# Kernel tuning notes

Measured on AMD Instinct MI355X. Metric: run time of the kernel, lower is better.

The kernel has to match this reference:

```python
import jax, jax.numpy as jnp
import numpy as np

B, C, T_IN, R, TB = 8192, 3, 2048, 64, 128
ALPHA = 10.0  # steepness of sigmoid surrogate spike
Q_INIT = 6.0


def surrogate_spike(x):
    # Differentiable surrogate for the spiking nonlinearity (sigmoid fast-spike).
    return jax.nn.sigmoid(ALPHA * x)


def setup_inputs() -> dict:
    key = jax.random.key(0)
    k0, k1 = jax.random.split(key)
    traces = jax.random.normal(k0, (B, C, T_IN), jnp.float32)
    drive_w = jax.random.normal(k1, (R, C), jnp.float32) / np.sqrt(C)
    drive_b = jnp.zeros((R,), jnp.float32)
    frequency_raw = jnp.linspace(-1.2, 1.2, R, dtype=jnp.float32)
    q_center = float(np.log(np.exp(max(Q_INIT - 1.5, 1e-3)) - 1.0))  # inverse softplus
    q_raw = jnp.full((R,), q_center, jnp.float32)
    threshold_raw = jnp.zeros((R,), jnp.float32)
    return dict(traces=traces, drive_w=drive_w, drive_b=drive_b,
                frequency_raw=frequency_raw, q_raw=q_raw, threshold_raw=threshold_raw)


def reference(traces, drive_w, drive_b, frequency_raw, q_raw, threshold_raw):
    b, c, t = traces.shape
    win = t // TB  # adaptive_avg_pool1d with evenly-dividing window
    pooled = traces.reshape(b, c, TB, win).mean(axis=-1)  # [B, C, TB]
    # _normalize_traces: divide by per-sample max-abs clamped to >= 1
    scale = jnp.maximum(jnp.max(jnp.abs(pooled), axis=(1, 2), keepdims=True), 1.0)
    pooled = pooled / scale
    # 1x1 Conv1d == per-timestep linear projection C -> R
    drive = jnp.einsum('bct,rc->brt', pooled, drive_w) + drive_b[None, :, None]  # [B, R, TB]

    frequency = 0.03 + 0.17 * jax.nn.sigmoid(frequency_raw)      # [R]
    q_factor = 1.5 + jax.nn.softplus(q_raw)                      # [R]
    decay = jnp.exp(-1.0 / q_factor)                             # [R]
    threshold = 0.35 + 0.75 * jax.nn.sigmoid(threshold_raw)      # [R]

    def step(carry, current):
        state, velocity = carry
        velocity = decay * velocity + current - frequency * state
        state = state + frequency * velocity
        spikes = surrogate_spike(state - threshold)
        state = state - spikes * threshold
        return (state, velocity), spikes

    init = (jnp.zeros((b, R), drive.dtype), jnp.zeros((b, R), drive.dtype))
    drive_t = jnp.moveaxis(drive, -1, 0)  # [TB, B, R]
    _, spike_seq = jax.lax.scan(step, init, drive_t)  # spike_seq: [TB, B, R]
    return spike_seq.mean(axis=0)  # [B, R]
```

## Files before the change

### kernel.cpp

```cpp
#include <hip/hip_runtime.h>
#include <math.h>

constexpr int kC   = 3;
constexpr int kTIn = 2048;
constexpr int kR   = 64;
constexpr int kTB  = 128;
constexpr float kAlpha = 10.0f;
constexpr float kLog2e = 1.44269504088896f;

constexpr int kK   = 4;
constexpr int kF4  = kC * kTIn / 4;

#ifndef __has_builtin
#define __has_builtin(x) 0
#endif

static __device__ __forceinline__ float fast_rcp(float x) {
#if __has_builtin(__builtin_amdgcn_rcpf)
    return __builtin_amdgcn_rcpf(x);
#else
    return 1.0f / x;
#endif
}

static __device__ __forceinline__ float fast_exp2(float x) {
#if __has_builtin(__builtin_amdgcn_exp2f)
    return __builtin_amdgcn_exp2f(x);
#else
    return __builtin_exp2f(x);
#endif
}

__global__ __launch_bounds__(256, 8)
void fused_encoder_kernel(const float* __restrict__ traces,
                          const float* __restrict__ drive_w,
                          const float* __restrict__ drive_b,
                          const float* __restrict__ freq_raw,
                          const float* __restrict__ q_raw,
                          const float* __restrict__ thr_raw,
                          float* __restrict__ out)
{
    __shared__ float sp[2][kTB * 4];
    __shared__ float red[2][3];

    const int tid  = threadIdx.x;
    const int wave = tid >> 6;
    const int lane = tid & 63;
    const int scanWave = blockIdx.x & 3;
    const long long base = (long long)blockIdx.x * kK;
    const float4* tr4 = reinterpret_cast<const float4*>(traces);

    if (wave != scanWave) {
        const int h = wave - (wave > scanWave ? 1 : 0);

        auto pool = [&](long long b, int buf) {
            const float4* src = tr4 + b * kF4 + (h * 8) * 64 + lane;
            float mloc = 0.0f;
            #pragma unroll
            for (int j = 0; j < 8; ++j) {
                float4 v = src[j * 64];
                float s = (v.x + v.y) + (v.z + v.w);
                s += __shfl_xor(s, 1, 64);
                s += __shfl_xor(s, 2, 64);
                mloc = fmaxf(mloc, fabsf(s));
                if ((lane & 3) == 0) {
                    int w = (h * 8 + j) * 16 + (lane >> 2);
                    sp[buf][(w & 127) * 4 + (w >> 7)] = s;
                }
            }
            #pragma unroll
            for (int off = 4; off <= 32; off <<= 1)
                mloc = fmaxf(mloc, __shfl_xor(mloc, off, 64));
            if (lane == 0) red[buf][h] = mloc;
        };

        pool(base, 0);
        __syncthreads();
        for (int k = 0; k < kK; ++k) {
            if (k + 1 < kK) pool(base + k + 1, (k + 1) & 1);
            __syncthreads();
        }
    } else {
        const int r = lane;
        const float w0   = drive_w[r * kC + 0];
        const float w1   = drive_w[r * kC + 1];
        const float w2   = drive_w[r * kC + 2];
        const float bias = drive_b[r];
        const float freq  = 0.03f + 0.17f / (1.0f + expf(-freq_raw[r]));
        const float qf    = 1.5f + log1pf(expf(q_raw[r]));
        const float decay = expf(-1.0f / qf);
        const float thr   = 0.35f + 0.75f / (1.0f + expf(-thr_raw[r]));
        const float expScale = kAlpha * kLog2e;
        const float thrE  = thr * expScale;

        __syncthreads();
        for (int k = 0; k < kK; ++k) {
            const int cur = k & 1;
            const float mm = fmaxf(fmaxf(red[cur][0], red[cur][1]), red[cur][2]);
            const float inv = fast_rcp(fmaxf(mm * (1.0f / 16.0f), 1.0f)) * (1.0f / 16.0f);
            const float v0 = w0 * inv, v1 = w1 * inv, v2 = w2 * inv;
            const float4* pt = reinterpret_cast<const float4*>(sp[cur]);

            __builtin_amdgcn_s_setprio(1);
            float state = 0.0f, vel = 0.0f, acc = 0.0f;
            #pragma unroll 8
            for (int t = 0; t < kTB; ++t) {
                float4 p = pt[t];
                float cur_ = fmaf(p.x, v0, bias);
                cur_ = fmaf(p.y, v1, cur_);
                cur_ = fmaf(p.z, v2, cur_);
                vel = fmaf(decay, vel, cur_);
                vel = fmaf(-freq, state, vel);
                state = fmaf(freq, vel, state);
                float e = fast_exp2(fmaf(-expScale, state, thrE));
                float spike = fast_rcp(1.0f + e);
                state = fmaf(-spike, thr, state);
                acc += spike;
            }
            __builtin_amdgcn_s_setprio(0);

            out[(base + k) * kR + r] = acc * (1.0f / kTB);
            __syncthreads();
        }
    }
}

extern "C" void kernel_launch(void* const* d_in, const int* in_sizes, int n_in,
                              void* d_out, int out_size, void* d_ws, size_t ws_size,
                              hipStream_t stream)
{
    const float* traces   = (const float*)d_in[0];
    const float* drive_w  = (const float*)d_in[1];
    const float* drive_b  = (const float*)d_in[2];
    const float* freq_raw = (const float*)d_in[3];
    const float* q_raw    = (const float*)d_in[4];
    const float* thr_raw  = (const float*)d_in[5];
    float* out = (float*)d_out;

    const int totalB = in_sizes[0] / (kC * kTIn);
    const int grid = totalB / kK;

    fused_encoder_kernel<<<grid, 256, 0, stream>>>(traces, drive_w, drive_b,
                                                   freq_raw, q_raw, thr_raw, out);
}
```

Measured before the change: 40.02 us.

## Split wave roles into two scan waves and two pooling waves per block

Each block now runs two scan waves and two pooling waves instead of one scan wave and three pooling waves. Each pooling wave reduces a whole sample, and the two scan waves handle alternate samples from a per-wave double-buffered shared tile. This halves the serial recurrence chain each block must run, which is the latency-bound critical path. In exchange, each pooling wave issues three times as many loads per sample, and shared memory use doubles.

```diff
diff --git a/kernel.cpp b/kernel.cpp
--- a/kernel.cpp
+++ b/kernel.cpp
@@ -40,32 +40,35 @@
                           const float* __restrict__ thr_raw,
                           float* __restrict__ out)
 {
-    __shared__ float sp[2][kTB * 4];
-    __shared__ float red[2][3];
+    __shared__ float sp[2][2][kTB * 4];
+    __shared__ float red[2][2];
 
     const int tid  = threadIdx.x;
     const int wave = tid >> 6;
     const int lane = tid & 63;
-    const int scanWave = blockIdx.x & 3;
+    const int s0 = blockIdx.x & 3;
+    const int s1 = s0 ^ 1;
     const long long base = (long long)blockIdx.x * kK;
     const float4* tr4 = reinterpret_cast<const float4*>(traces);
 
-    if (wave != scanWave) {
-        const int h = wave - (wave > scanWave ? 1 : 0);
+    const bool isScan = (wave == s0) || (wave == s1);
+
+    if (!isScan) {
+        const int h = wave & 1;
 
         auto pool = [&](long long b, int buf) {
-            const float4* src = tr4 + b * kF4 + (h * 8) * 64 + lane;
+            const float4* src = tr4 + b * kF4 + lane;
             float mloc = 0.0f;
             #pragma unroll
-            for (int j = 0; j < 8; ++j) {
+            for (int j = 0; j < 24; ++j) {
                 float4 v = src[j * 64];
                 float s = (v.x + v.y) + (v.z + v.w);
                 s += __shfl_xor(s, 1, 64);
                 s += __shfl_xor(s, 2, 64);
                 mloc = fmaxf(mloc, fabsf(s));
                 if ((lane & 3) == 0) {
-                    int w = (h * 8 + j) * 16 + (lane >> 2);
-                    sp[buf][(w & 127) * 4 + (w >> 7)] = s;
+                    int w = j * 16 + (lane >> 2);
+                    sp[buf][h][(w & 127) * 4 + (w >> 7)] = s;
                 }
             }
             #pragma unroll
@@ -74,13 +77,14 @@
             if (lane == 0) red[buf][h] = mloc;
         };
 
-        pool(base, 0);
+        pool(base + h, 0);
         __syncthreads();
-        for (int k = 0; k < kK; ++k) {
-            if (k + 1 < kK) pool(base + k + 1, (k + 1) & 1);
+        for (int p = 0; p < 2; ++p) {
+            if (p + 1 < 2) pool(base + 2 * (p + 1) + h, (p + 1) & 1);
             __syncthreads();
         }
     } else {
+        const int si = (wave == s1) ? 1 : 0;
         const int r = lane;
         const float w0   = drive_w[r * kC + 0];
         const float w1   = drive_w[r * kC + 1];
@@ -94,21 +98,21 @@
         const float thrE  = thr * expScale;
 
         __syncthreads();
-        for (int k = 0; k < kK; ++k) {
-            const int cur = k & 1;
-            const float mm = fmaxf(fmaxf(red[cur][0], red[cur][1]), red[cur][2]);
+        for (int p = 0; p < 2; ++p) {
+            const int cur = p & 1;
+            const float mm = red[cur][si];
             const float inv = fast_rcp(fmaxf(mm * (1.0f / 16.0f), 1.0f)) * (1.0f / 16.0f);
             const float v0 = w0 * inv, v1 = w1 * inv, v2 = w2 * inv;
-            const float4* pt = reinterpret_cast<const float4*>(sp[cur]);
+            const float4* pt = reinterpret_cast<const float4*>(sp[cur][si]);
 
             __builtin_amdgcn_s_setprio(1);
             float state = 0.0f, vel = 0.0f, acc = 0.0f;
             #pragma unroll 8
             for (int t = 0; t < kTB; ++t) {
-                float4 p = pt[t];
-                float cur_ = fmaf(p.x, v0, bias);
-                cur_ = fmaf(p.y, v1, cur_);
-                cur_ = fmaf(p.z, v2, cur_);
+                float4 pv = pt[t];
+                float cur_ = fmaf(pv.x, v0, bias);
+                cur_ = fmaf(pv.y, v1, cur_);
+                cur_ = fmaf(pv.z, v2, cur_);
                 vel = fmaf(decay, vel, cur_);
                 vel = fmaf(-freq, state, vel);
                 state = fmaf(freq, vel, state);
@@ -119,7 +123,7 @@
             }
             __builtin_amdgcn_s_setprio(0);
 
-            out[(base + k) * kR + r] = acc * (1.0f / kTB);
+            out[(base + 2 * p + si) * kR + r] = acc * (1.0f / kTB);
             __syncthreads();
         }
     }
```

After: 49.55 us. 23.8% more time.

## Persistent grid with async global-to-LDS double-buffered trace loading

Applied to the files above, without the earlier changes.

Switches to a fixed 768-block persistent grid in which each block handles a contiguous range of samples. Raw traces now go straight into LDS through async global_load_lds, double-buffered two samples ahead, and are pooled from shared memory. Synchronisation uses manual s_waitcnt and s_barrier. The aim is to keep more bytes in flight and overlap the memory-bound load with the sequential scan. The cost is large LDS use (about 48KB per block), lower occupancy, and a longer serial scan chain in each block's scan wave.

```diff
diff --git a/kernel.cpp b/kernel.cpp
--- a/kernel.cpp
+++ b/kernel.cpp
@@ -8,8 +8,8 @@
 constexpr float kAlpha = 10.0f;
 constexpr float kLog2e = 1.44269504088896f;
 
-constexpr int kK   = 4;
-constexpr int kF4  = kC * kTIn / 4;
+constexpr int kSampleF = kC * kTIn;
+constexpr int kGrid    = 768;
 
 #ifndef __has_builtin
 #define __has_builtin(x) 0
@@ -31,54 +31,81 @@
 #endif
 }
 
-__global__ __launch_bounds__(256, 8)
+__global__ __launch_bounds__(256, 3)
 void fused_encoder_kernel(const float* __restrict__ traces,
                           const float* __restrict__ drive_w,
                           const float* __restrict__ drive_b,
                           const float* __restrict__ freq_raw,
                           const float* __restrict__ q_raw,
                           const float* __restrict__ thr_raw,
-                          float* __restrict__ out)
+                          float* __restrict__ out,
+                          int kSmall, int rem)
 {
+    __shared__ float raw[2][kSampleF];
     __shared__ float sp[2][kTB * 4];
     __shared__ float red[2][3];
 
     const int tid  = threadIdx.x;
     const int wave = tid >> 6;
     const int lane = tid & 63;
-    const int scanWave = blockIdx.x & 3;
-    const long long base = (long long)blockIdx.x * kK;
-    const float4* tr4 = reinterpret_cast<const float4*>(traces);
 
-    if (wave != scanWave) {
-        const int h = wave - (wave > scanWave ? 1 : 0);
+    const int bx = blockIdx.x;
+    int K; long long base;
+    if (bx < rem) { K = kSmall + 1; base = (long long)bx * K; }
+    else          { K = kSmall;     base = (long long)rem * (kSmall + 1)
+                                         + (long long)(bx - rem) * kSmall; }
 
-        auto pool = [&](long long b, int buf) {
-            const float4* src = tr4 + b * kF4 + (h * 8) * 64 + lane;
+    if (wave < 3) {
+        const int p = wave;
+
+        auto dma = [&](long long s, int buf) {
+            const float* src = traces + s * kSampleF + p * 2048 + lane * 4;
+            float* dst = &raw[buf][p * 2048];
+            #pragma unroll
+            for (int j = 0; j < 8; ++j) {
+                __builtin_amdgcn_global_load_lds(
+                    (const __attribute__((address_space(1))) void*)(src + j * 256),
+                    (__attribute__((address_space(3))) void*)(dst + j * 256),
+                    16, 0, 0);
+            }
+        };
+        auto pool = [&](int buf) {
+            const float4* r4 = reinterpret_cast<const float4*>(raw[buf]);
             float mloc = 0.0f;
             #pragma unroll
-            for (int j = 0; j < 8; ++j) {
-                float4 v = src[j * 64];
+            for (int j2 = 0; j2 < 8; ++j2) {
+                const int j = p * 8 + j2;
+                float4 v = r4[j * 64 + lane];
                 float s = (v.x + v.y) + (v.z + v.w);
                 s += __shfl_xor(s, 1, 64);
                 s += __shfl_xor(s, 2, 64);
                 mloc = fmaxf(mloc, fabsf(s));
                 if ((lane & 3) == 0) {
-                    int w = (h * 8 + j) * 16 + (lane >> 2);
+                    int w = j * 16 + (lane >> 2);
                     sp[buf][(w & 127) * 4 + (w >> 7)] = s;
                 }
             }
             #pragma unroll
             for (int off = 4; off <= 32; off <<= 1)
                 mloc = fmaxf(mloc, __shfl_xor(mloc, off, 64));
-            if (lane == 0) red[buf][h] = mloc;
+            if (lane == 0) red[buf][p] = mloc;
         };
 
-        pool(base, 0);
-        __syncthreads();
-        for (int k = 0; k < kK; ++k) {
-            if (k + 1 < kK) pool(base + k + 1, (k + 1) & 1);
-            __syncthreads();
+        dma(base + 0, 0);
+        if (K > 1) dma(base + 1, 1);
+        asm volatile("s_waitcnt vmcnt(8)" ::: "memory");
+        pool(0);
+        asm volatile("s_waitcnt lgkmcnt(0)\n\ts_barrier" ::: "memory");
+
+        for (int k = 0; k < K; ++k) {
+            if (k + 2 < K) {
+                dma(base + k + 2, k & 1);
+                asm volatile("s_waitcnt vmcnt(8)" ::: "memory");
+            } else {
+                asm volatile("s_waitcnt vmcnt(0)" ::: "memory");
+            }
+            if (k + 1 < K) pool((k + 1) & 1);
+            asm volatile("s_waitcnt lgkmcnt(0)\n\ts_barrier" ::: "memory");
         }
     } else {
         const int r = lane;
@@ -93,8 +120,8 @@
         const float expScale = kAlpha * kLog2e;
         const float thrE  = thr * expScale;
 
-        __syncthreads();
-        for (int k = 0; k < kK; ++k) {
+        asm volatile("s_barrier" ::: "memory");
+        for (int k = 0; k < K; ++k) {
             const int cur = k & 1;
             const float mm = fmaxf(fmaxf(red[cur][0], red[cur][1]), red[cur][2]);
             const float inv = fast_rcp(fmaxf(mm * (1.0f / 16.0f), 1.0f)) * (1.0f / 16.0f);
@@ -105,10 +132,10 @@
             float state = 0.0f, vel = 0.0f, acc = 0.0f;
             #pragma unroll 8
             for (int t = 0; t < kTB; ++t) {
-                float4 p = pt[t];
-                float cur_ = fmaf(p.x, v0, bias);
-                cur_ = fmaf(p.y, v1, cur_);
-                cur_ = fmaf(p.z, v2, cur_);
+                float4 pv = pt[t];
+                float cur_ = fmaf(pv.x, v0, bias);
+                cur_ = fmaf(pv.y, v1, cur_);
+                cur_ = fmaf(pv.z, v2, cur_);
                 vel = fmaf(decay, vel, cur_);
                 vel = fmaf(-freq, state, vel);
                 state = fmaf(freq, vel, state);
@@ -120,7 +147,7 @@
             __builtin_amdgcn_s_setprio(0);
 
             out[(base + k) * kR + r] = acc * (1.0f / kTB);
-            __syncthreads();
+            asm volatile("s_barrier" ::: "memory");
         }
     }
 }
@@ -137,9 +164,11 @@
     const float* thr_raw  = (const float*)d_in[5];
     float* out = (float*)d_out;
 
-    const int totalB = in_sizes[0] / (kC * kTIn);
-    const int grid = totalB / kK;
+    const int totalB = in_sizes[0] / kSampleF;
+    const int kSmall = totalB / kGrid;
+    const int rem    = totalB % kGrid;
 
-    fused_encoder_kernel<<<grid, 256, 0, stream>>>(traces, drive_w, drive_b,
-                                                   freq_raw, q_raw, thr_raw, out);
+    fused_encoder_kernel<<<kGrid, 256, 0, stream>>>(traces, drive_w, drive_b,
+                                                    freq_raw, q_raw, thr_raw,
+                                                    out, kSmall, rem);
 }
```

After: 60.29 us. +50.6%, slower.
